# Optimization experiments

Hardware: AMD Instinct MI355X
Metric: run time of the kernel (lower is better)

## Reference

```python
import jax, jax.numpy as jnp
import numpy as np

B, N, D_MODEL = 2, 4096, 2048
H = 4
KEY_DIM = 1024          # d_model * 0.5
DK = KEY_DIM // H       # 256, head_qk_dim
DV = D_MODEL // H       # 512, head_v_dim
CHUNK = 64
EPS = 1e-5


def setup_inputs() -> dict:
    key = jax.random.key(0)
    ks = jax.random.split(key, 6)
    s = 0.02  # small init scale, mimics xavier-ish magnitude
    return {
        "x": jax.random.normal(ks[0], (B, N, D_MODEL), jnp.float32),
        "Wq": jax.random.normal(ks[1], (KEY_DIM, D_MODEL), jnp.float32) * s,
        "Wk": jax.random.normal(ks[2], (KEY_DIM, D_MODEL), jnp.float32) * s,
        "Wv": jax.random.normal(ks[3], (D_MODEL, D_MODEL), jnp.float32) * s,
        "Wg": jax.random.normal(ks[4], (D_MODEL, D_MODEL), jnp.float32) * s,
        "Wo": jax.random.normal(ks[5], (D_MODEL, D_MODEL), jnp.float32) * s,
        "gnorm_w": jnp.ones((DV,), jnp.float32),
    }


def _rope(qk):
    # non-interleaved rotary over full head dim; qk: [b, n, h, d]
    n, d = qk.shape[1], qk.shape[3]
    inv_freq = 1.0 / (10000.0 ** (jnp.arange(0, d, 2, dtype=jnp.float32) / d))
    freqs = jnp.arange(n, dtype=jnp.float32)[:, None] * inv_freq[None, :]  # [n, d/2]
    cos = jnp.cos(freqs)[None, :, None, :]
    sin = jnp.sin(freqs)[None, :, None, :]
    x1, x2 = qk[..., : d // 2], qk[..., d // 2 :]
    return jnp.concatenate([x1 * cos - x2 * sin, x2 * cos + x1 * sin], axis=-1)


def _retention_forward(x, Wq, Wk, Wv, Wg, Wo, gnorm_w):
    b, n, dm = x.shape
    dk, dv = Wq.shape[0] // H, Wv.shape[0] // H
    q = (x @ Wq.T).reshape(b, n, H, dk)
    k = (x @ Wk.T).reshape(b, n, H, dk)
    q, k = _rope(q), _rope(k)
    v = (x @ Wv.T).reshape(b, n, H, dv)
    # -> [b, h, n, d]
    q = q.transpose(0, 2, 1, 3) * (dk ** -0.5)
    k = k.transpose(0, 2, 1, 3)
    v = v.transpose(0, 2, 1, 3)

    # multi-scale decay: gamma_h = 1 - 2^(-5-h)
    gamma = 1.0 - jnp.exp2(-5.0 - jnp.arange(H, dtype=jnp.float32))  # [H]

    C = CHUNK
    nc = n // C
    qc = q.reshape(b, H, nc, C, dk).transpose(2, 0, 1, 3, 4)  # [nc,b,H,C,dk]
    kc = k.reshape(b, H, nc, C, dk).transpose(2, 0, 1, 3, 4)
    vc = v.reshape(b, H, nc, C, dv).transpose(2, 0, 1, 3, 4)

    i = jnp.arange(C)
    expo = (i[:, None] - i[None, :]).astype(jnp.float32)          # i - j
    dmask = jnp.where(expo >= 0, gamma[:, None, None] ** expo, 0.0)  # [H,C,C]
    g_in = gamma[:, None] ** (i + 1).astype(jnp.float32)          # [H,C] cross-chunk decay
    g_k = gamma[:, None] ** (C - 1 - i).astype(jnp.float32)       # [H,C] state-update decay
    g_C = gamma ** C                                               # [H]

    def step(S, inp):
        qi, ki, vi = inp  # [b,H,C,dk], [b,H,C,dk], [b,H,C,dv]
        attn = jnp.einsum('bhid,bhjd->bhij', qi, ki) * dmask[None]
        o_intra = jnp.einsum('bhij,bhjv->bhiv', attn, vi)
        o_inter = jnp.einsum('bhid,bhdv->bhiv', qi, S) * g_in[None, :, :, None]
        S_new = S * g_C[None, :, None, None] + jnp.einsum(
            'bhjd,bhjv->bhdv', ki * g_k[None, :, :, None], vi)
        return S_new, o_intra + o_inter

    S0 = jnp.zeros((b, H, dk, dv), x.dtype)
    _, oc = jax.lax.scan(step, S0, (qc, kc, vc))          # oc: [nc,b,H,C,dv]
    o = oc.transpose(1, 0, 3, 2, 4).reshape(b, n, H, dv)  # [b,n,h,dv]

    # per-head RMSNorm (group_norm over head_v_dim)
    o = o * jax.lax.rsqrt(jnp.mean(o * o, axis=-1, keepdims=True) + EPS) * gnorm_w

    g = jax.nn.silu(x @ Wg.T)  # [b,n,d_model]
    return (o.reshape(b, n, H * dv) * g) @ Wo.T


def reference(x, Wq, Wk, Wv, Wg, Wo, gnorm_w):
    return _retention_forward(x, Wq, Wk, Wv, Wg, Wo, gnorm_w)
```

## Files before the change

kernel.cpp:

```cpp
#include <hip/hip_runtime.h>
#include <hip/hip_bf16.h>
#include <stdint.h>

constexpr int Bb   = 2;
constexpr int Nn   = 4096;
constexpr int DM   = 2048;
constexpr int Hh   = 4;
constexpr int DK   = 256;
constexpr int DV   = 512;
constexpr int QKS  = 2048;
constexpr int CH   = 64;
constexpr int NC   = Nn / CH;
constexpr int M    = Bb * Nn;

typedef __attribute__((ext_vector_type(8))) short s16x8;
typedef __attribute__((ext_vector_type(4))) float f32x4;

__device__ __forceinline__ float b2f(uint16_t h) {
  return __uint_as_float(((uint32_t)h) << 16);
}
__device__ __forceinline__ uint16_t f2b(float f) {
  uint32_t u = __float_as_uint(f);
  return (uint16_t)((u + 0x7fffu + ((u >> 16) & 1u)) >> 16);
}

__device__ __forceinline__ void gload16(const void* g, void* l) {
  __builtin_amdgcn_global_load_lds(
      (const __attribute__((address_space(1))) void*)g,
      (__attribute__((address_space(3))) void*)l, 16, 0, 0);
}

#define BARRIER()  asm volatile("s_barrier" ::: "memory")
#define WAITLGKM() do { asm volatile("s_waitcnt lgkmcnt(0)" ::: "memory"); \
                        __builtin_amdgcn_sched_barrier(0); } while (0)
#define VMCNT4()   asm volatile("s_waitcnt vmcnt(4)" ::: "memory")
#define VMCNT0()   asm volatile("s_waitcnt vmcnt(0)" ::: "memory")

__global__ __launch_bounds__(256) void conv_f2b(const float* __restrict__ s,
                                                uint16_t* __restrict__ d, int n8) {
  int i = blockIdx.x * 256 + threadIdx.x;
  if (i >= n8) return;
  const float4* sp = (const float4*)s;
  float4 a = sp[2 * i], b = sp[2 * i + 1];
  uint4 o;
  o.x = (uint32_t)f2b(a.x) | ((uint32_t)f2b(a.y) << 16);
  o.y = (uint32_t)f2b(a.z) | ((uint32_t)f2b(a.w) << 16);
  o.z = (uint32_t)f2b(b.x) | ((uint32_t)f2b(b.y) << 16);
  o.w = (uint32_t)f2b(b.z) | ((uint32_t)f2b(b.w) << 16);
  ((uint4*)d)[i] = o;
}

__global__ __launch_bounds__(256) void conv_w4(const float* __restrict__ Wq,
                                               const float* __restrict__ Wk,
                                               const float* __restrict__ Wv,
                                               const float* __restrict__ Wg,
                                               uint16_t* __restrict__ dst) {
  const int i = blockIdx.x * 256 + threadIdx.x;
  const float* s; int off;
  if (i < 262144)       { s = Wq; off = i; }
  else if (i < 524288)  { s = Wk; off = i - 262144; }
  else if (i < 1048576) { s = Wv; off = i - 524288; }
  else                  { s = Wg; off = i - 1048576; }
  const float4* sp = (const float4*)s;
  float4 a = sp[2 * off], b = sp[2 * off + 1];
  uint4 o;
  o.x = (uint32_t)f2b(a.x) | ((uint32_t)f2b(a.y) << 16);
  o.y = (uint32_t)f2b(a.z) | ((uint32_t)f2b(a.w) << 16);
  o.z = (uint32_t)f2b(b.x) | ((uint32_t)f2b(b.y) << 16);
  o.w = (uint32_t)f2b(b.z) | ((uint32_t)f2b(b.w) << 16);
  ((uint4*)dst)[i] = o;
}

__global__ __launch_bounds__(512) void gemm_fused3(const uint16_t* __restrict__ A,
                                                   const uint16_t* __restrict__ W,
                                                   uint16_t* __restrict__ out0,
                                                   int K) {
  __shared__ uint16_t Al[2][2][8192];
  __shared__ uint16_t Bl[2][2][8192];
  const int tid = threadIdx.x;
  const int l = tid & 63, w = tid >> 6;
  const int wm = w >> 2, wn = w & 3;
  const int m0 = blockIdx.x * 256, n0 = blockIdx.y * 256;
  const int fr = l & 15;
  const int pu = (((l >> 4) ^ ((fr >> 1) & 3)) * 8);
  const int ssw = ((l & 3) ^ ((l >> 3) & 3)) * 8;
  const uint16_t* aS = A + (size_t)(m0 + w * 32 + (l >> 2)) * K + ssw;
  const uint16_t* wS = W + (size_t)(n0 + w * 32 + (l >> 2)) * K + ssw;

  f32x4 acc[8][4];
#pragma unroll
  for (int mi = 0; mi < 8; ++mi)
#pragma unroll
    for (int nj = 0; nj < 4; ++nj) {
      f32x4 z = {0.f, 0.f, 0.f, 0.f};
      acc[mi][nj] = z;
    }

#define STG_A(S, KH, KT) do {                                                \
    const uint16_t* _p = aS + (size_t)(KT) * 64 + (KH) * 32;                 \
    gload16(_p,                   &Al[S][KH][(w * 32) * 32]);                \
    gload16(_p + (size_t)16 * K,  &Al[S][KH][(w * 32 + 16) * 32]);           \
  } while (0)
#define STG_B(S, KH, KT) do {                                                \
    const uint16_t* _p = wS + (size_t)(KT) * 64 + (KH) * 32;                 \
    gload16(_p,                   &Bl[S][KH][(w * 32) * 32]);                \
    gload16(_p + (size_t)16 * K,  &Bl[S][KH][(w * 32 + 16) * 32]);           \
  } while (0)
#define LDA(S, KH, MI) (*(const s16x8*)&Al[S][KH][(wm * 128 + (MI) * 16 + fr) * 32 + pu])
#define LDB(S, KH, NJ) (*(const s16x8*)&Bl[S][KH][(wn * 64 + (NJ) * 16 + fr) * 32 + pu])
#define MFMA16(Q) do {                                                       \
    __builtin_amdgcn_s_setprio(1);                                           \
    _Pragma("unroll")                                                        \
    for (int mi = 0; mi < 8; ++mi)                                           \
      acc[mi][2*(Q)] = __builtin_amdgcn_mfma_f32_16x16x32_bf16(              \
          aF[mi], bF0, acc[mi][2*(Q)], 0, 0, 0);                             \
    _Pragma("unroll")                                                        \
    for (int mi = 0; mi < 8; ++mi)                                           \
      acc[mi][2*(Q)+1] = __builtin_amdgcn_mfma_f32_16x16x32_bf16(            \
          aF[mi], bF1, acc[mi][2*(Q)+1], 0, 0, 0);                           \
    __builtin_amdgcn_s_setprio(0);                                           \
  } while (0)

  STG_A(0, 0, 0); STG_B(0, 0, 0); STG_A(0, 1, 0); STG_B(0, 1, 0);
  STG_A(1, 0, 1); STG_B(1, 0, 1);
  VMCNT0();
  BARRIER();

  const int NI = K / 128;
  s16x8 aF[8], bF0, bF1;

  for (int i = 0; i < NI; ++i) {
    const bool nl = (i < NI - 1);
    const size_t t1 = 2 * i + 1, t2 = 2 * i + 2, t3 = 2 * i + 3;
#pragma unroll
    for (int mi = 0; mi < 8; ++mi) aF[mi] = LDA(0, 0, mi);
    bF0 = LDB(0, 0, 0); bF1 = LDB(0, 0, 1);
    STG_A(1, 1, t1);
    BARRIER(); WAITLGKM(); MFMA16(0); BARRIER();
    bF0 = LDB(0, 0, 2); bF1 = LDB(0, 0, 3);
    STG_B(1, 1, t1);
    BARRIER(); WAITLGKM(); MFMA16(1); BARRIER();
#pragma unroll
    for (int mi = 0; mi < 8; ++mi) aF[mi] = LDA(0, 1, mi);
    bF0 = LDB(0, 1, 0); bF1 = LDB(0, 1, 1);
    if (nl) STG_A(0, 0, t2);
    BARRIER(); WAITLGKM(); MFMA16(0); BARRIER();
    bF0 = LDB(0, 1, 2); bF1 = LDB(0, 1, 3);
    if (nl) STG_B(0, 0, t2);
    BARRIER(); WAITLGKM(); MFMA16(1);
    if (nl) VMCNT4(); else VMCNT0();
    BARRIER();
#pragma unroll
    for (int mi = 0; mi < 8; ++mi) aF[mi] = LDA(1, 0, mi);
    bF0 = LDB(1, 0, 0); bF1 = LDB(1, 0, 1);
    if (nl) STG_A(0, 1, t2);
    BARRIER(); WAITLGKM(); MFMA16(0); BARRIER();
    bF0 = LDB(1, 0, 2); bF1 = LDB(1, 0, 3);
    if (nl) STG_B(0, 1, t2);
    BARRIER(); WAITLGKM(); MFMA16(1); BARRIER();
#pragma unroll
    for (int mi = 0; mi < 8; ++mi) aF[mi] = LDA(1, 1, mi);
    bF0 = LDB(1, 1, 0); bF1 = LDB(1, 1, 1);
    if (nl) STG_A(1, 0, t3);
    BARRIER(); WAITLGKM(); MFMA16(0); BARRIER();
    bF0 = LDB(1, 1, 2); bF1 = LDB(1, 1, 3);
    if (nl) STG_B(1, 0, t3);
    BARRIER(); WAITLGKM(); MFMA16(1);
    VMCNT4();
    BARRIER();
  }
#undef STG_A
#undef STG_B
#undef LDA
#undef LDB
#undef MFMA16

  uint16_t* Cb = out0 + (size_t)(n0 >> 11) * 16777216;
  const int r0 = m0 + wm * 128 + (l >> 4) * 4;
  const int c0 = (n0 & 2047) + wn * 64 + fr;
#pragma unroll
  for (int mi = 0; mi < 8; ++mi)
#pragma unroll
    for (int nj = 0; nj < 4; ++nj)
#pragma unroll
      for (int p = 0; p < 4; ++p) {
        const int row = r0 + mi * 16 + p;
        const int col = c0 + nj * 16;
        Cb[(size_t)row * 2048 + col] = f2b(acc[mi][nj][p]);
      }
}

__global__ __launch_bounds__(512, 2) void gemm_fin(const uint16_t* __restrict__ A,
                                                   const uint16_t* __restrict__ W,
                                                   float* __restrict__ C,
                                                   int Nd, int K) {
  __shared__ uint16_t As[3][256 * 32];
  __shared__ uint16_t Bs[3][128 * 32];
  const int tid = threadIdx.x;
  const int l = tid & 63, w = tid >> 6;
  const int wm = w >> 2, wn = w & 3;
  const int m0 = blockIdx.x * 256, n0 = blockIdx.y * 128;
  const int fr = l & 15, fk = (l >> 4) * 8;
  const int fkA = fk ^ ((fr & 3) << 3);
  const int sk = ((tid & 3) ^ ((tid >> 2) & 3)) * 8;
  const uint16_t* aP = A + (size_t)(m0 + w * 16 + (l >> 2)) * K + sk;
  const uint16_t* wP = W + (size_t)(n0 + w * 16 + (l >> 2)) * K + sk;

  f32x4 acc[8][2];
#pragma unroll
  for (int mi = 0; mi < 8; ++mi)
#pragma unroll
    for (int nj = 0; nj < 2; ++nj) {
      f32x4 z = {0.f, 0.f, 0.f, 0.f};
      acc[mi][nj] = z;
    }

#define STAGEF(T, BUF)                                                       \
  {                                                                          \
    const size_t k0_ = (size_t)(T) * 32;                                     \
    uint16_t* as_ = &As[BUF][w * 512];                                       \
    gload16(aP + k0_, as_);                                                  \
    gload16(aP + (size_t)128 * K + k0_, as_ + 4096);                         \
    gload16(wP + k0_, &Bs[BUF][w * 512]);                                    \
  }

  const int NT = K / 32;
  STAGEF(0, 0);
  STAGEF(1, 1);
  for (int t = 0; t < NT; ++t) {
    if (t < NT - 1) asm volatile("s_waitcnt vmcnt(3)" ::: "memory");
    else            asm volatile("s_waitcnt vmcnt(0)" ::: "memory");
    __builtin_amdgcn_s_barrier();
    __builtin_amdgcn_sched_barrier(0);
    if (t + 2 < NT) STAGEF(t + 2, (t + 2) % 3);
    const int cur = t % 3;
    s16x8 af[8], bf2[2];
    const uint16_t* Ab = &As[cur][(wm * 128 + fr) * 32 + fkA];
    const uint16_t* Bp = &Bs[cur][(wn * 32 + fr) * 32 + fkA];
#pragma unroll
    for (int mi = 0; mi < 8; ++mi) af[mi] = *(const s16x8*)(Ab + mi * 512);
#pragma unroll
    for (int nj = 0; nj < 2; ++nj) bf2[nj] = *(const s16x8*)(Bp + nj * 512);
    __builtin_amdgcn_s_setprio(1);
#pragma unroll
    for (int mi = 0; mi < 8; ++mi)
#pragma unroll
      for (int nj = 0; nj < 2; ++nj)
        acc[mi][nj] = __builtin_amdgcn_mfma_f32_16x16x32_bf16(af[mi], bf2[nj],
                                                              acc[mi][nj], 0, 0, 0);
    __builtin_amdgcn_s_setprio(0);
  }
#undef STAGEF

  const int r0 = m0 + wm * 128 + (l >> 4) * 4;
  const int c0 = n0 + wn * 32 + fr;
#pragma unroll
  for (int mi = 0; mi < 8; ++mi)
#pragma unroll
    for (int nj = 0; nj < 2; ++nj)
#pragma unroll
      for (int p = 0; p < 4; ++p)
        C[(size_t)(r0 + mi * 16 + p) * Nd + c0 + nj * 16] = acc[mi][nj][p];
}

__global__ void rope_kernel(uint16_t* __restrict__ qk) {
  const int idx = blockIdx.x * 256 + threadIdx.x;
  const int i = idx & 127;
  const int h = (idx >> 7) & 3;
  const int n = (idx >> 9) & (Nn - 1);
  const int b = idx >> 21;
  const size_t base = ((size_t)(b * Nn + n)) * QKS + h * DK;
  const float invf = (float)exp((double)i * -0.071955784156063938);
  const float theta = (float)n * invf;
  float sn, cs;
  sincosf(theta, &sn, &cs);
  float x1 = b2f(qk[base + i]), x2 = b2f(qk[base + 128 + i]);
  qk[base + i]       = f2b((x1 * cs - x2 * sn) * 0.0625f);
  qk[base + 128 + i] = f2b((x2 * cs + x1 * sn) * 0.0625f);
  x1 = b2f(qk[base + 1024 + i]); x2 = b2f(qk[base + 1024 + 128 + i]);
  qk[base + 1024 + i]       = f2b(x1 * cs - x2 * sn);
  qk[base + 1024 + 128 + i] = f2b(x2 * cs + x1 * sn);
}

__global__ __launch_bounds__(256) void transpose_v(const uint16_t* __restrict__ v,
                                                   uint16_t* __restrict__ vt) {
  const int nt = blockIdx.x & 63;
  const int wt = (blockIdx.x >> 6) & 7;
  const int bh = blockIdx.x >> 9;
  const int b = bh >> 2, h = bh & 3;
  __shared__ uint16_t t[64][72];
  const int lr = threadIdx.x >> 2, lc = (threadIdx.x & 3) * 16;
  const uint16_t* src = v + ((size_t)(b * Nn + nt * 64 + lr)) * DM + h * DV + wt * 64 + lc;
  *(uint4*)&t[lr][lc]     = *(const uint4*)src;
  *(uint4*)&t[lr][lc + 8] = *(const uint4*)(src + 8);
  __syncthreads();
  uint16_t out[16];
#pragma unroll
  for (int e = 0; e < 16; ++e) out[e] = t[lc + e][lr];
  uint16_t* dst = vt + ((size_t)bh * 512 + wt * 64 + lr) * 4096 + nt * 64 + lc;
  *(uint4*)dst       = *(uint4*)&out[0];
  *(uint4*)(dst + 8) = *(uint4*)&out[8];
}

__global__ __launch_bounds__(256) void transpose_k(const uint16_t* __restrict__ qk,
                                                   uint16_t* __restrict__ kt) {
  const int nt = blockIdx.x & 63;
  const int dt = (blockIdx.x >> 6) & 3;
  const int bh = blockIdx.x >> 8;
  const int b = bh >> 2, h = bh & 3;
  __shared__ uint16_t t[64][72];
  const int lr = threadIdx.x >> 2, lc = (threadIdx.x & 3) * 16;
  const uint16_t* src = qk + ((size_t)(b * Nn + nt * 64 + lr)) * QKS + 1024 + h * DK + dt * 64 + lc;
  *(uint4*)&t[lr][lc]     = *(const uint4*)src;
  *(uint4*)&t[lr][lc + 8] = *(const uint4*)(src + 8);
  __syncthreads();
  const float l2g = log2f(1.f - exp2f(-5.f - (float)h));
  uint16_t out[16];
#pragma unroll
  for (int e = 0; e < 16; ++e)
    out[e] = f2b(b2f(t[lc + e][lr]) * exp2f((float)(63 - (lc + e)) * l2g));
  uint16_t* dst = kt + ((size_t)bh * 256 + dt * 64 + lr) * 4096 + nt * 64 + lc;
  *(uint4*)dst       = *(uint4*)&out[0];
  *(uint4*)(dst + 8) = *(uint4*)&out[8];
}

__global__ __launch_bounds__(256) void attn_mfma(const uint16_t* __restrict__ qk,
                                                 uint16_t* __restrict__ attn) {
  const int c  = blockIdx.x & 63;
  const int bh = blockIdx.x >> 6;
  const int b = bh >> 2, h = bh & 3;
  const int tid = threadIdx.x;
  const int l = tid & 63, w = tid >> 6;
  const int fr = l & 15, fk = (l >> 4) * 8;
  const int n0 = c * CH;
  const uint16_t* qbase = qk + ((size_t)(b * Nn + n0)) * QKS + h * DK;
  const uint16_t* kbase = qbase + 1024;
  f32x4 acc[4];
#pragma unroll
  for (int nj = 0; nj < 4; ++nj) {
    f32x4 z = {0.f, 0.f, 0.f, 0.f};
    acc[nj] = z;
  }
#pragma unroll
  for (int ks = 0; ks < 8; ++ks) {
    s16x8 qf = *(const s16x8*)(qbase + (size_t)(w * 16 + fr) * QKS + ks * 32 + fk);
    s16x8 kf[4];
#pragma unroll
    for (int nj = 0; nj < 4; ++nj)
      kf[nj] = *(const s16x8*)(kbase + (size_t)(nj * 16 + fr) * QKS + ks * 32 + fk);
#pragma unroll
    for (int nj = 0; nj < 4; ++nj)
      acc[nj] = __builtin_amdgcn_mfma_f32_16x16x32_bf16(qf, kf[nj], acc[nj], 0, 0, 0);
  }
  const float l2g = log2f(1.f - exp2f(-5.f - (float)h));
  uint16_t* ab = attn + ((size_t)bh * 64 + c) * 4096;
  const int rbase = (l >> 4) * 4;
#pragma unroll
  for (int pp = 0; pp < 4; ++pp) {
    const int i = w * 16 + rbase + pp;
#pragma unroll
    for (int nj = 0; nj < 4; ++nj) {
      const int j = nj * 16 + fr;
      const float val = (i >= j) ? acc[nj][pp] * exp2f((float)(i - j) * l2g) : 0.f;
      ab[(size_t)i * 64 + j] = f2b(val);
    }
  }
}

__global__ __launch_bounds__(256) void chunk_outer(const uint16_t* __restrict__ kt,
                                                   const uint16_t* __restrict__ vt,
                                                   uint16_t* __restrict__ U, int p) {
  const int c  = blockIdx.x & 63;
  const int bh = blockIdx.x >> 6;
  const int tid = threadIdx.x;
  const int l = tid & 63, w = tid >> 6;
  const int wrow = (w >> 1) * 64;
  const int wcol = (w & 1) * 128;
  const int fr = l & 15, fk = (l >> 4) * 8;
  const int n0 = c * CH;
  const uint16_t* vtb = vt + ((size_t)bh * 512 + p * 128) * 4096 + n0;
  const uint16_t* ktb = kt + ((size_t)bh * 256) * 4096 + n0;
  f32x4 acc[4][8];
#pragma unroll
  for (int mi = 0; mi < 4; ++mi)
#pragma unroll
    for (int nj = 0; nj < 8; ++nj) {
      f32x4 z = {0.f, 0.f, 0.f, 0.f};
      acc[mi][nj] = z;
    }
#pragma unroll
  for (int ks = 0; ks < 2; ++ks) {
    s16x8 af[4], bf8[8];
#pragma unroll
    for (int mi = 0; mi < 4; ++mi)
      af[mi] = *(const s16x8*)(vtb + (size_t)(wrow + mi * 16 + fr) * 4096 + ks * 32 + fk);
#pragma unroll
    for (int nj = 0; nj < 8; ++nj)
      bf8[nj] = *(const s16x8*)(ktb + (size_t)(wcol + nj * 16 + fr) * 4096 + ks * 32 + fk);
#pragma unroll
    for (int mi = 0; mi < 4; ++mi)
#pragma unroll
      for (int nj = 0; nj < 8; ++nj)
        acc[mi][nj] = __builtin_amdgcn_mfma_f32_16x16x32_bf16(af[mi], bf8[nj],
                                                              acc[mi][nj], 0, 0, 0);
  }
  uint16_t* Ub = U + (size_t)bh * 2097152 + (size_t)c * 32768;
  const int rbase = (l >> 4) * 4;
#pragma unroll
  for (int mi = 0; mi < 4; ++mi)
#pragma unroll
    for (int nj = 0; nj < 8; ++nj)
#pragma unroll
      for (int pp = 0; pp < 4; ++pp) {
        const int wq = wrow + mi * 16 + rbase + pp;
        const int d  = wcol + nj * 16 + fr;
        Ub[(size_t)wq * 256 + d] = f2b(acc[mi][nj][pp]);
      }
}

__global__ __launch_bounds__(256) void state_scan(uint16_t* __restrict__ U) {
  const int gid = blockIdx.x * 256 + threadIdx.x;
  const int bh = gid >> 15;
  const int e  = gid & 32767;
  const int h  = bh & 3;
  const float l2g = log2f(1.f - exp2f(-5.f - (float)h));
  const float gC = exp2f(64.f * l2g);
  uint16_t* p = U + (size_t)bh * 2097152 + e;
  float S = 0.f;
  for (int cb = 0; cb < 8; ++cb) {
    uint16_t* base = p + (size_t)cb * 8 * 32768;
    float u[8];
#pragma unroll
    for (int ee = 0; ee < 8; ++ee) u[ee] = b2f(base[(size_t)ee * 32768]);
#pragma unroll
    for (int ee = 0; ee < 8; ++ee) {
      base[(size_t)ee * 32768] = f2b(S);
      S = gC * S + u[ee];
    }
  }
}

__global__ __launch_bounds__(256) void scan_out(const uint16_t* __restrict__ qk,
                                                const uint16_t* __restrict__ vt,
                                                const uint16_t* __restrict__ attn,
                                                const uint16_t* __restrict__ U,
                                                uint16_t* __restrict__ o, int p) {
  const int c  = blockIdx.x & 63;
  const int bh = blockIdx.x >> 6;
  const int b = bh >> 2, h = bh & 3;
  const int tid = threadIdx.x;
  const int l = tid & 63, wv = tid >> 6;
  const int wcol = wv * 32;
  const int fr = l & 15, fk = (l >> 4) * 8;
  const int n0 = c * CH;
  f32x4 aQS[4][2], aPV[4][2];
#pragma unroll
  for (int mi = 0; mi < 4; ++mi)
#pragma unroll
    for (int nj = 0; nj < 2; ++nj) {
      f32x4 z = {0.f, 0.f, 0.f, 0.f};
      aQS[mi][nj] = z; aPV[mi][nj] = z;
    }
  const uint16_t* qbase = qk + ((size_t)(b * Nn + n0)) * QKS + h * DK;
  const uint16_t* Ub = U + (size_t)bh * 2097152 + (size_t)c * 32768;
#pragma unroll
  for (int ks = 0; ks < 8; ++ks) {
    s16x8 qf[4], sf[2];
#pragma unroll
    for (int mi = 0; mi < 4; ++mi)
      qf[mi] = *(const s16x8*)(qbase + (size_t)(mi * 16 + fr) * QKS + ks * 32 + fk);
#pragma unroll
    for (int nj = 0; nj < 2; ++nj)
      sf[nj] = *(const s16x8*)(Ub + (size_t)(wcol + nj * 16 + fr) * 256 + ks * 32 + fk);
#pragma unroll
    for (int mi = 0; mi < 4; ++mi)
#pragma unroll
      for (int nj = 0; nj < 2; ++nj)
        aQS[mi][nj] = __builtin_amdgcn_mfma_f32_16x16x32_bf16(qf[mi], sf[nj],
                                                              aQS[mi][nj], 0, 0, 0);
  }
  const uint16_t* ab = attn + ((size_t)bh * 64 + c) * 4096;
  const uint16_t* vtb = vt + ((size_t)bh * 512 + p * 128) * 4096 + n0;
#pragma unroll
  for (int ks = 0; ks < 2; ++ks) {
    s16x8 af[4], vf[2];
#pragma unroll
    for (int mi = 0; mi < 4; ++mi)
      af[mi] = *(const s16x8*)(ab + (size_t)(mi * 16 + fr) * 64 + ks * 32 + fk);
#pragma unroll
    for (int nj = 0; nj < 2; ++nj)
      vf[nj] = *(const s16x8*)(vtb + (size_t)(wcol + nj * 16 + fr) * 4096 + ks * 32 + fk);
#pragma unroll
    for (int mi = 0; mi < 4; ++mi)
#pragma unroll
      for (int nj = 0; nj < 2; ++nj)
        aPV[mi][nj] = __builtin_amdgcn_mfma_f32_16x16x32_bf16(af[mi], vf[nj],
                                                              aPV[mi][nj], 0, 0, 0);
  }
  const float l2g = log2f(1.f - exp2f(-5.f - (float)h));
  const int rbase = (l >> 4) * 4;
#pragma unroll
  for (int mi = 0; mi < 4; ++mi)
#pragma unroll
    for (int pp = 0; pp < 4; ++pp) {
      const int i = mi * 16 + rbase + pp;
      const float gi = exp2f((float)(i + 1) * l2g);
#pragma unroll
      for (int nj = 0; nj < 2; ++nj) {
        const int wc_ = wcol + nj * 16 + fr;
        const float val = aPV[mi][nj][pp] + gi * aQS[mi][nj][pp];
        o[((size_t)(b * Nn + n0 + i)) * DM + h * DV + p * 128 + wc_] = f2b(val);
      }
    }
}

__global__ __launch_bounds__(256) void gn_gate(const uint16_t* __restrict__ o,
                                               uint16_t* __restrict__ g,
                                               const float* __restrict__ gw) {
  const int bn = blockIdx.x;
  const int tid = threadIdx.x;
  const int h = tid >> 6;
  const int lane = tid & 63;
  const size_t base = (size_t)bn * DM + h * DV + lane * 8;
  uint4 ov4 = *(const uint4*)&o[base];
  float ov[8] = { b2f((uint16_t)ov4.x), b2f((uint16_t)(ov4.x >> 16)),
                  b2f((uint16_t)ov4.y), b2f((uint16_t)(ov4.y >> 16)),
                  b2f((uint16_t)ov4.z), b2f((uint16_t)(ov4.z >> 16)),
                  b2f((uint16_t)ov4.w), b2f((uint16_t)(ov4.w >> 16)) };
  float ss = 0.f;
#pragma unroll
  for (int e = 0; e < 8; ++e) ss += ov[e] * ov[e];
#pragma unroll
  for (int m = 1; m < 64; m <<= 1) ss += __shfl_xor(ss, m, 64);
  const float r = rsqrtf(ss * (1.f / 512.f) + 1e-5f);
  uint4 gv = *(const uint4*)&g[base];
  float gf[8] = { b2f((uint16_t)gv.x), b2f((uint16_t)(gv.x >> 16)),
                  b2f((uint16_t)gv.y), b2f((uint16_t)(gv.y >> 16)),
                  b2f((uint16_t)gv.z), b2f((uint16_t)(gv.z >> 16)),
                  b2f((uint16_t)gv.w), b2f((uint16_t)(gv.w >> 16)) };
  const float* gwp = gw + lane * 8;
  uint16_t res[8];
#pragma unroll
  for (int e = 0; e < 8; ++e) {
    float sil = gf[e] / (1.f + expf(-gf[e]));
    res[e] = f2b(ov[e] * r * gwp[e] * sil);
  }
  uint4 outv;
  outv.x = (uint32_t)res[0] | ((uint32_t)res[1] << 16);
  outv.y = (uint32_t)res[2] | ((uint32_t)res[3] << 16);
  outv.z = (uint32_t)res[4] | ((uint32_t)res[5] << 16);
  outv.w = (uint32_t)res[6] | ((uint32_t)res[7] << 16);
  *(uint4*)&g[base] = outv;
}

extern "C" void kernel_launch(void* const* d_in, const int* in_sizes, int n_in,
                              void* d_out, int out_size, void* d_ws, size_t ws_size,
                              hipStream_t stream) {
  const float* x  = (const float*)d_in[0];
  const float* Wq = (const float*)d_in[1];
  const float* Wk = (const float*)d_in[2];
  const float* Wv = (const float*)d_in[3];
  const float* Wg = (const float*)d_in[4];
  const float* Wo = (const float*)d_in[5];
  const float* gw = (const float*)d_in[6];

  char* base = (char*)d_ws;
  uint16_t* xb   = (uint16_t*)(base);
  uint16_t* U    = (uint16_t*)(base);
  uint16_t* qkb  = (uint16_t*)(base + ((size_t)32 << 20));
  uint16_t* vb   = (uint16_t*)(base + ((size_t)64 << 20));
  uint16_t* kt   = (uint16_t*)(base + ((size_t)64 << 20));
  uint16_t* attn = (uint16_t*)(base + ((size_t)80 << 20));
  uint16_t* wob  = (uint16_t*)(base + ((size_t)84 << 20));
  uint16_t* gb   = (uint16_t*)(base + ((size_t)96 << 20));
  uint16_t* wall = (uint16_t*)(base + ((size_t)128 << 20));
  uint16_t* vt   = (uint16_t*)(base + ((size_t)128 << 20));
  uint16_t* qb   = qkb;
  uint16_t* o16  = (uint16_t*)d_out;

  dim3 blk(256), blkG(512);
  conv_f2b<<<dim3(8192), blk, 0, stream>>>(x, xb, M * DM / 8);
  conv_w4<<<dim3(6144), blk, 0, stream>>>(Wq, Wk, Wv, Wg, wall);
  gemm_fused3<<<dim3(M/256, 6144/256), blkG, 0, stream>>>(xb, wall, qkb, DM);
  rope_kernel<<<dim3((Bb*Nn*Hh*128)/256), blk, 0, stream>>>(qkb);
  transpose_v<<<dim3(8*8*64), blk, 0, stream>>>(vb, vt);
  conv_f2b<<<dim3(2048), blk, 0, stream>>>(Wo, wob, DM * DM / 8);
  transpose_k<<<dim3(8*4*64), blk, 0, stream>>>(qkb, kt);
  attn_mfma<<<dim3(Bb*Hh*NC), blk, 0, stream>>>(qkb, attn);
  for (int p = 0; p < 4; ++p) {
    chunk_outer<<<dim3(Bb*Hh*NC),  blk, 0, stream>>>(kt, vt, U, p);
    state_scan<<<dim3(1024),       blk, 0, stream>>>(U);
    scan_out<<<dim3(Bb*Hh*NC),     blk, 0, stream>>>(qb, vt, attn, U, o16, p);
  }
  gn_gate<<<dim3(M), blk, 0, stream>>>(o16, gb, gw);
  gemm_fin<<<dim3(M/256, DM/128), blkG, 0, stream>>>(gb, wob, (float*)d_out, DM, DM);
}
```

Baseline: 549.0 us.

## Restructure final GEMM into 4-phase pingpong pipeline with 64-wide K tiles

Rewrites the output-projection GEMM's main loop. The 3-stage ring of 32-wide K buffers becomes two stages of 64-wide K tiles, each split into two 32-halves, with loads issued per half-phase between barriers and vmcnt waits. It also changes the LDS swizzle and the global load mapping, and drops the 2-blocks-per-CU launch bound. The aim is to overlap global-to-LDS traffic with MFMA work at finer grain and cut barrier stalls, at the cost of more barriers per iteration and possibly lower occupancy.

Measured after the change: 559.7 us. Within noise of the previous version (+2.0%).

```diff
diff --git a/kernel.cpp b/kernel.cpp
--- a/kernel.cpp
+++ b/kernel.cpp
@@ -33,7 +33,9 @@
 #define BARRIER()  asm volatile("s_barrier" ::: "memory")
 #define WAITLGKM() do { asm volatile("s_waitcnt lgkmcnt(0)" ::: "memory"); \
                         __builtin_amdgcn_sched_barrier(0); } while (0)
+#define VMCNT6()   asm volatile("s_waitcnt vmcnt(6)" ::: "memory")
 #define VMCNT4()   asm volatile("s_waitcnt vmcnt(4)" ::: "memory")
+#define VMCNT3()   asm volatile("s_waitcnt vmcnt(3)" ::: "memory")
 #define VMCNT0()   asm volatile("s_waitcnt vmcnt(0)" ::: "memory")
 
 __global__ __launch_bounds__(256) void conv_f2b(const float* __restrict__ s,
@@ -190,21 +192,21 @@
       }
 }
 
-__global__ __launch_bounds__(512, 2) void gemm_fin(const uint16_t* __restrict__ A,
-                                                   const uint16_t* __restrict__ W,
-                                                   float* __restrict__ C,
-                                                   int Nd, int K) {
-  __shared__ uint16_t As[3][256 * 32];
-  __shared__ uint16_t Bs[3][128 * 32];
+__global__ __launch_bounds__(512) void gemm_fin(const uint16_t* __restrict__ A,
+                                                const uint16_t* __restrict__ W,
+                                                float* __restrict__ C,
+                                                int Nd, int K) {
+  __shared__ uint16_t Al[2][2][8192];
+  __shared__ uint16_t Bl[2][2][4096];
   const int tid = threadIdx.x;
   const int l = tid & 63, w = tid >> 6;
   const int wm = w >> 2, wn = w & 3;
   const int m0 = blockIdx.x * 256, n0 = blockIdx.y * 128;
-  const int fr = l & 15, fk = (l >> 4) * 8;
-  const int fkA = fk ^ ((fr & 3) << 3);
-  const int sk = ((tid & 3) ^ ((tid >> 2) & 3)) * 8;
-  const uint16_t* aP = A + (size_t)(m0 + w * 16 + (l >> 2)) * K + sk;
-  const uint16_t* wP = W + (size_t)(n0 + w * 16 + (l >> 2)) * K + sk;
+  const int fr = l & 15;
+  const int pu = (((l >> 4) ^ ((fr >> 1) & 3)) * 8);
+  const int ssw = ((l & 3) ^ ((l >> 3) & 3)) * 8;
+  const uint16_t* aS = A + (size_t)(m0 + w * 32 + (l >> 2)) * K + ssw;
+  const uint16_t* wS = W + (size_t)(n0 + w * 16 + (l >> 2)) * K + ssw;
 
   f32x4 acc[8][2];
 #pragma unroll
@@ -215,42 +217,69 @@
       acc[mi][nj] = z;
     }
 
-#define STAGEF(T, BUF)                                                       \
-  {                                                                          \
-    const size_t k0_ = (size_t)(T) * 32;                                     \
-    uint16_t* as_ = &As[BUF][w * 512];                                       \
-    gload16(aP + k0_, as_);                                                  \
-    gload16(aP + (size_t)128 * K + k0_, as_ + 4096);                         \
-    gload16(wP + k0_, &Bs[BUF][w * 512]);                                    \
-  }
-
-  const int NT = K / 32;
-  STAGEF(0, 0);
-  STAGEF(1, 1);
-  for (int t = 0; t < NT; ++t) {
-    if (t < NT - 1) asm volatile("s_waitcnt vmcnt(3)" ::: "memory");
-    else            asm volatile("s_waitcnt vmcnt(0)" ::: "memory");
-    __builtin_amdgcn_s_barrier();
-    __builtin_amdgcn_sched_barrier(0);
-    if (t + 2 < NT) STAGEF(t + 2, (t + 2) % 3);
-    const int cur = t % 3;
-    s16x8 af[8], bf2[2];
-    const uint16_t* Ab = &As[cur][(wm * 128 + fr) * 32 + fkA];
-    const uint16_t* Bp = &Bs[cur][(wn * 32 + fr) * 32 + fkA];
-#pragma unroll
-    for (int mi = 0; mi < 8; ++mi) af[mi] = *(const s16x8*)(Ab + mi * 512);
-#pragma unroll
-    for (int nj = 0; nj < 2; ++nj) bf2[nj] = *(const s16x8*)(Bp + nj * 512);
-    __builtin_amdgcn_s_setprio(1);
-#pragma unroll
-    for (int mi = 0; mi < 8; ++mi)
-#pragma unroll
-      for (int nj = 0; nj < 2; ++nj)
-        acc[mi][nj] = __builtin_amdgcn_mfma_f32_16x16x32_bf16(af[mi], bf2[nj],
-                                                              acc[mi][nj], 0, 0, 0);
-    __builtin_amdgcn_s_setprio(0);
-  }
-#undef STAGEF
+#define FSTG(S, KH, KT) do {                                                 \
+    const uint16_t* _pa = aS + (size_t)(KT) * 64 + (KH) * 32;                \
+    gload16(_pa,                  &Al[S][KH][(w * 32) * 32]);                \
+    gload16(_pa + (size_t)16 * K, &Al[S][KH][(w * 32 + 16) * 32]);           \
+    const uint16_t* _pb = wS + (size_t)(KT) * 64 + (KH) * 32;                \
+    gload16(_pb,                  &Bl[S][KH][(w * 16) * 32]);                \
+  } while (0)
+#define FLDA(S, KH, MI) (*(const s16x8*)&Al[S][KH][(wm * 128 + (MI) * 16 + fr) * 32 + pu])
+#define FLDB(S, KH, NJ) (*(const s16x8*)&Bl[S][KH][(wn * 32 + (NJ) * 16 + fr) * 32 + pu])
+#define FPHASE(RS, RKH) do {                                                 \
+    _Pragma("unroll")                                                        \
+    for (int mi = 0; mi < 8; ++mi) aF[mi] = FLDA(RS, RKH, mi);               \
+    bF0 = FLDB(RS, RKH, 0); bF1 = FLDB(RS, RKH, 1);                          \
+  } while (0)
+#define FMFMA() do {                                                         \
+    __builtin_amdgcn_s_setprio(1);                                           \
+    _Pragma("unroll")                                                        \
+    for (int mi = 0; mi < 8; ++mi)                                           \
+      acc[mi][0] = __builtin_amdgcn_mfma_f32_16x16x32_bf16(                  \
+          aF[mi], bF0, acc[mi][0], 0, 0, 0);                                 \
+    _Pragma("unroll")                                                        \
+    for (int mi = 0; mi < 8; ++mi)                                           \
+      acc[mi][1] = __builtin_amdgcn_mfma_f32_16x16x32_bf16(                  \
+          aF[mi], bF1, acc[mi][1], 0, 0, 0);                                 \
+    __builtin_amdgcn_s_setprio(0);                                           \
+  } while (0)
+
+  FSTG(0, 0, 0); FSTG(0, 1, 0); FSTG(1, 0, 1);
+  VMCNT0();
+  BARRIER();
+
+  const int NI = K / 128;
+  s16x8 aF[8], bF0, bF1;
+
+  for (int i = 0; i < NI; ++i) {
+    const bool nl = (i < NI - 1);
+    const size_t t1 = 2 * i + 1, t2 = 2 * i + 2, t3 = 2 * i + 3;
+    FPHASE(0, 0);
+    FSTG(1, 1, t1);
+    BARRIER(); WAITLGKM(); FMFMA();
+    VMCNT6();
+    BARRIER();
+    FPHASE(0, 1);
+    if (nl) FSTG(0, 0, t2);
+    BARRIER(); WAITLGKM(); FMFMA();
+    if (nl) VMCNT6(); else VMCNT3();
+    BARRIER();
+    FPHASE(1, 0);
+    if (nl) FSTG(0, 1, t2);
+    BARRIER(); WAITLGKM(); FMFMA();
+    if (nl) VMCNT6(); else VMCNT0();
+    BARRIER();
+    FPHASE(1, 1);
+    if (nl) FSTG(1, 0, t3);
+    BARRIER(); WAITLGKM(); FMFMA();
+    if (nl) VMCNT6();
+    BARRIER();
+  }
+#undef FSTG
+#undef FLDA
+#undef FLDB
+#undef FPHASE
+#undef FMFMA
 
   const int r0 = m0 + wm * 128 + (l >> 4) * 4;
   const int c0 = n0 + wn * 32 + fr;
```
